# Kernel optimization log

Measured on AMD Instinct MI355X. Metric: run time of the kernel, lower is better.

The kernel has to match this reference:

```python
import jax, jax.numpy as jnp
import numpy as np

N_NODES = 50000
N_EDGES = 800000
VOCAB = 32000
IN_FEATS = 128
N_HIDDEN = 128
N_CLASSES = 40
SEQ_LEN = 20
PAD_IX = 0


def setup_inputs() -> dict:
    key = jax.random.key(0)
    ks = jax.random.split(key, 6)
    features = jax.random.randint(ks[0], (N_NODES, SEQ_LEN), 0, VOCAB, dtype=jnp.int64 if jax.config.jax_enable_x64 else jnp.int32).astype(jnp.int32)
    src = jax.random.randint(ks[1], (N_EDGES,), 0, N_NODES, dtype=jnp.int32)
    dst = jax.random.randint(ks[2], (N_EDGES,), 0, N_NODES, dtype=jnp.int32)
    emb_weight = jax.random.normal(ks[3], (VOCAB, IN_FEATS), dtype=jnp.float32) * 0.02
    emb_weight = emb_weight.at[PAD_IX].set(0.0)  # padding_idx row is zero
    W1 = jax.random.normal(ks[4], (IN_FEATS, N_HIDDEN), dtype=jnp.float32) * (1.0 / np.sqrt(IN_FEATS))
    b1 = jnp.zeros((N_HIDDEN,), dtype=jnp.float32)
    W2 = jax.random.normal(ks[5], (N_HIDDEN, N_CLASSES), dtype=jnp.float32) * (1.0 / np.sqrt(N_HIDDEN))
    b2 = jnp.zeros((N_CLASSES,), dtype=jnp.float32)
    return {"features": features, "src": src, "dst": dst, "emb_weight": emb_weight,
            "W1": W1, "b1": b1, "W2": W2, "b2": b2}


def _graph_conv(h, src, dst, W, b, n_nodes, activation=None):
    # DGL GraphConv with norm='both': D_out^{-1/2} applied to src feats,
    # sum-aggregate along edges, D_in^{-1/2} on dst, then linear (+bias, act).
    ones = jnp.ones(src.shape[0], dtype=h.dtype)
    out_deg = jax.ops.segment_sum(ones, src, num_segments=n_nodes)
    in_deg = jax.ops.segment_sum(ones, dst, num_segments=n_nodes)
    h = h * jax.lax.rsqrt(jnp.maximum(out_deg, 1.0))[:, None]
    agg = jax.ops.segment_sum(h[src], dst, num_segments=n_nodes)  # gather + scatter-add (SpMM)
    agg = agg * jax.lax.rsqrt(jnp.maximum(in_deg, 1.0))[:, None]
    out = agg @ W + b
    if activation is not None:
        out = activation(out)
    return out


def reference(features, src, dst, emb_weight, W1, b1, W2, b2):
    n_nodes = features.shape[0]
    # embedding mean-pool over non-pad tokens: [n_nodes, seq, d] -> [n_nodes, d]
    seq_len = jnp.maximum(jnp.sum(features != PAD_IX, axis=1, keepdims=True), 1).astype(emb_weight.dtype)
    h = jnp.take(emb_weight, features, axis=0).sum(axis=1) / seq_len
    h = _graph_conv(h, src, dst, W1, b1, n_nodes, activation=jax.nn.relu)
    # dropout is identity in eval mode
    h = _graph_conv(h, src, dst, W2, b2, n_nodes)
    return h
```

## Files before the change

### kernel.cpp

```cpp
#include <hip/hip_runtime.h>
#include <math.h>

#define N_NODES 50000
#define N_EDGES 800000
#define IN_FEATS 128
#define N_HIDDEN 128
#define N_CLASSES 40
#define SEQ_LEN 20
#define VOCAB 32000
#define BUCKET_CAP 64

#define NPART 196
#define PCAP 4608
#define EGS_BLOCKS 892
#define POOL_BLOCKS 12500
#define PREP_BLOCKS 89
#define GEMM2_BLOCKS 782

typedef __attribute__((ext_vector_type(8))) short bf16x8;
typedef __attribute__((ext_vector_type(4))) float f32x4;

#define AS1 __attribute__((address_space(1)))
#define AS3 __attribute__((address_space(3)))

__device__ __forceinline__ void gld_lds16(const void* g, void* l) {
    __builtin_amdgcn_global_load_lds((const AS1 unsigned int*)g,
                                     (AS3 unsigned int*)l, 16, 0, 0);
}
__device__ __forceinline__ void vm_wait0() {
    asm volatile("s_waitcnt vmcnt(0)" ::: "memory");
}

__device__ inline unsigned short f2bf(float x) {
    union { float f; unsigned int u; } v; v.f = x;
    unsigned int r = v.u + 0x7FFF + ((v.u >> 16) & 1);
    return (unsigned short)(r >> 16);
}
__device__ inline float bf2f(unsigned short b) {
    union { float f; unsigned int u; } v; v.u = ((unsigned int)b) << 16;
    return v.f;
}


__global__ __launch_bounds__(256) void prep_kernel(
        int4* __restrict__ pcnt_zero, const float* __restrict__ W1,
        unsigned short* __restrict__ W1p, const float* __restrict__ W2,
        unsigned short* __restrict__ W2p) {
    int b = blockIdx.x;
    int t = threadIdx.x;
    if (b == 0) {
        if (t < 128) pcnt_zero[t] = make_int4(0, 0, 0, 0);
    } else if (b < 65) {
        int i = (b - 1) * 256 + t;
        int tile = i >> 9, rem = i & 511;
        int ln = rem >> 3, j = rem & 7;
        int nt = tile >> 2, kb = tile & 3;
        int k = kb * 32 + ((ln >> 4) << 3) + j;
        int n = nt * 16 + (ln & 15);
        W1p[i] = f2bf(W1[k * 128 + n]);
    } else {
        int i = (b - 65) * 256 + t;
        int tile = i >> 9, rem = i & 511;
        int ln = rem >> 3, j = rem & 7;
        int nt = tile >> 2, kb = tile & 3;
        int k = kb * 32 + ((ln >> 4) << 3) + j;
        int n = nt * 16 + (ln & 15);
        W2p[i] = (n < N_CLASSES) ? f2bf(W2[k * N_CLASSES + n]) : (unsigned short)0;
    }
}

__global__ __launch_bounds__(256) void egemm_scat_kernel(
        const int* __restrict__ src, const int* __restrict__ dst,
        unsigned int* __restrict__ pcnt_s, unsigned char* __restrict__ pbuf_s,
        unsigned int* __restrict__ pcnt_d, unsigned int* __restrict__ pbuf_d,
        const float* __restrict__ emb, const unsigned short* __restrict__ W1p,
        unsigned short* __restrict__ Ep) {
    __shared__ unsigned int shm[512];
    int b = blockIdx.x;
    int t = threadIdx.x;
    if (b < 196) {
        unsigned int* lhist = shm;
        unsigned int* lbase = shm + 256;
        for (int i = t; i < NPART; i += 256) lhist[i] = 0u;
        __syncthreads();
        int base = b * 4096;
        int pid[16]; unsigned int rank[16]; unsigned char val[16];
        #pragma unroll
        for (int k = 0; k < 16; ++k) {
            int i = base + k * 256 + t;
            pid[k] = -1;
            if (i < N_EDGES) {
                int u = src[i];
                val[k] = (unsigned char)(u & 255);
                pid[k] = u >> 8;
                rank[k] = atomicAdd(&lhist[pid[k]], 1u);
            }
        }
        __syncthreads();
        for (int i = t; i < NPART; i += 256)
            lbase[i] = atomicAdd(&pcnt_s[i], lhist[i]);
        __syncthreads();
        #pragma unroll
        for (int k = 0; k < 16; ++k) {
            if (pid[k] >= 0) {
                unsigned int pos = lbase[pid[k]] + rank[k];
                if (pos < PCAP) pbuf_s[pid[k] * PCAP + pos] = val[k];
            }
        }
    } else if (b < 392) {
        unsigned int* lhist = shm;
        unsigned int* lbase = shm + 256;
        for (int i = t; i < NPART; i += 256) lhist[i] = 0u;
        __syncthreads();
        int base = (b - 196) * 4096;
        int pid[16]; unsigned int rank[16]; unsigned int val[16];
        #pragma unroll
        for (int k = 0; k < 16; ++k) {
            int i = base + k * 256 + t;
            pid[k] = -1;
            if (i < N_EDGES) {
                int u = src[i];
                int d = dst[i];
                val[k] = ((unsigned int)u << 8) | (unsigned int)(d & 255);
                pid[k] = d >> 8;
                rank[k] = atomicAdd(&lhist[pid[k]], 1u);
            }
        }
        __syncthreads();
        for (int i = t; i < NPART; i += 256)
            lbase[i] = atomicAdd(&pcnt_d[i], lhist[i]);
        __syncthreads();
        #pragma unroll
        for (int k = 0; k < 16; ++k) {
            if (pid[k] >= 0) {
                unsigned int pos = lbase[pid[k]] + rank[k];
                if (pos < PCAP) pbuf_d[pid[k] * PCAP + pos] = val[k];
            }
        }
    } else {
        const int wave = t >> 6, lane = t & 63;
        const int quad = lane >> 4, m = lane & 15;
        const int row0 = (b - 392) * 64 + wave * 16;
        const int arow = row0 + m;
        const float4* ap = (const float4*)(emb + arow * 128 + quad * 8);
        bf16x8 a[4];
        #pragma unroll
        for (int kb = 0; kb < 4; ++kb) {
            float4 x = ap[kb * 8];
            float4 y = ap[kb * 8 + 1];
            bf16x8 tt;
            tt[0] = f2bf(x.x); tt[1] = f2bf(x.y); tt[2] = f2bf(x.z); tt[3] = f2bf(x.w);
            tt[4] = f2bf(y.x); tt[5] = f2bf(y.y); tt[6] = f2bf(y.z); tt[7] = f2bf(y.w);
            a[kb] = tt;
        }
        const int rbase = row0 + quad * 4;
        #pragma unroll
        for (int nt = 0; nt < 8; ++nt) {
            const unsigned short* wp = W1p + (nt * 4) * 512 + lane * 8;
            bf16x8 b0 = *(const bf16x8*)(wp + 0 * 512);
            bf16x8 b1 = *(const bf16x8*)(wp + 1 * 512);
            bf16x8 b2 = *(const bf16x8*)(wp + 2 * 512);
            bf16x8 b3 = *(const bf16x8*)(wp + 3 * 512);
            f32x4 acc = {0.f, 0.f, 0.f, 0.f};
            acc = __builtin_amdgcn_mfma_f32_16x16x32_bf16(a[0], b0, acc, 0, 0, 0);
            acc = __builtin_amdgcn_mfma_f32_16x16x32_bf16(a[1], b1, acc, 0, 0, 0);
            acc = __builtin_amdgcn_mfma_f32_16x16x32_bf16(a[2], b2, acc, 0, 0, 0);
            acc = __builtin_amdgcn_mfma_f32_16x16x32_bf16(a[3], b3, acc, 0, 0, 0);
            #pragma unroll
            for (int r = 0; r < 4; ++r)
                Ep[(rbase + r) * 128 + nt * 16 + m] = f2bf(acc[r]);
        }
    }
}

__global__ __launch_bounds__(256) void count_kernel(
        const unsigned int* __restrict__ pcnt_s, const unsigned char* __restrict__ pbuf_s,
        const unsigned int* __restrict__ pcnt_d, const unsigned int* __restrict__ pbuf_d,
        unsigned int* __restrict__ cnt, float* __restrict__ routf,
        unsigned short* __restrict__ bucketu) {
    __shared__ unsigned int ho[256];
    __shared__ unsigned int hi_[256];
    int p = blockIdx.x, t = threadIdx.x;
    ho[t] = 0u;
    hi_[t] = 0u;
    __syncthreads();
    int ns = min((int)pcnt_s[p], PCAP);
    const unsigned char* ps = pbuf_s + p * PCAP;
    for (int i = t; i < ns; i += 256) atomicAdd(&ho[ps[i]], 1u);
    int nd = min((int)pcnt_d[p], PCAP);
    const unsigned int* pd = pbuf_d + p * PCAP;
    for (int i = t; i < nd; i += 256) {
        unsigned int e = pd[i];
        unsigned int d = e & 255u;
        unsigned int slot = atomicAdd(&hi_[d], 1u);
        if (slot < BUCKET_CAP)
            bucketu[(p * 256 + (int)d) * BUCKET_CAP + slot] = (unsigned short)(e >> 8);
    }
    __syncthreads();
    int v = p * 256 + t;
    if (v < N_NODES) {
        cnt[v] = (ho[t] << 16) | (hi_[t] & 0xffffu);
        routf[v] = rsqrtf(fmaxf((float)ho[t], 1.f));
    }
}

__global__ __launch_bounds__(256) void pool_kernel(
        const float* __restrict__ routf, const int* __restrict__ feats,
        const unsigned short* __restrict__ Ep, unsigned short* __restrict__ G1) {
    __shared__ unsigned int pstage[4][SEQ_LEN][64];
    __shared__ int tokl[4][SEQ_LEN];
    int t = threadIdx.x;
    int w = t >> 6, lane = t & 63;
    int v = blockIdx.x * 4 + w;
    int mytok = 0;
    if (lane < SEQ_LEN) {
        mytok = feats[v * SEQ_LEN + lane];
        tokl[w][lane] = mytok;
    }
    int nz = (int)__popcll(__ballot(lane < SEQ_LEN && mytok != 0));
    __syncthreads();
    #pragma unroll
    for (int g = 0; g < SEQ_LEN / 4; ++g) {
        int tok = tokl[w][4 * g + (lane >> 4)];
        gld_lds16(Ep + tok * 128 + (lane & 15) * 8, &pstage[w][4 * g][0]);
    }
    float ro = routf[v];
    vm_wait0();
    float a0 = 0.f, a1 = 0.f;
    #pragma unroll
    for (int s = 0; s < SEQ_LEN; ++s) {
        unsigned int x = pstage[w][s][lane];
        a0 += bf2f((unsigned short)(x & 0xffffu));
        a1 += bf2f((unsigned short)(x >> 16));
    }
    float sc = ro / (float)max(nz, 1);
    ushort2 o = {f2bf(a0 * sc), f2bf(a1 * sc)};
    ((ushort2*)G1)[v * 64 + lane] = o;
}

__global__ __launch_bounds__(256) void spmm1_kernel(
        const unsigned int* __restrict__ cnt, const float* __restrict__ routf,
        const unsigned short* __restrict__ bucketu, const unsigned short* __restrict__ G,
        const float* __restrict__ b1, unsigned short* __restrict__ h1) {
    __shared__ unsigned short idxs[256];
    __shared__ unsigned int stg[4][32][64];
    int t = threadIdx.x;
    int node = t >> 6, lane = t & 63;
    int v = blockIdx.x * 4 + node;
    idxs[t] = bucketu[blockIdx.x * 256 + t];
    int ind = (int)(cnt[v] & 0xffffu);
    float rov = routf[v];
    float2 bb = ((const float2*)b1)[lane];
    int n = min(ind, BUCKET_CAP);
    float a0 = 0.f, a1 = 0.f;
    for (int base = 0; base < n; base += 32) {
        int m = min(32, n - base);
        int nin = (m + 3) >> 2;
        for (int g = 0; g < nin; ++g) {
            int rc = min(base + 4 * g + (lane >> 4), n - 1);
            int u = idxs[node * 64 + rc];
            gld_lds16(G + u * 128 + (lane & 15) * 8, &stg[node][4 * g][0]);
        }
        vm_wait0();
        #pragma unroll 4
        for (int j = 0; j < m; ++j) {
            unsigned int x = stg[node][j][lane];
            a0 += bf2f((unsigned short)(x & 0xffffu));
            a1 += bf2f((unsigned short)(x >> 16));
        }
    }
    float rin = rsqrtf(fmaxf((float)ind, 1.f));
    float v0 = fmaxf(a0 * rin + bb.x, 0.f) * rov;
    float v1 = fmaxf(a1 * rin + bb.y, 0.f) * rov;
    ushort2 o = {f2bf(v0), f2bf(v1)};
    ((ushort2*)h1)[v * 64 + lane] = o;
}

__global__ __launch_bounds__(256) void gemm2_kernel(
        const unsigned short* __restrict__ h1, const unsigned short* __restrict__ W2p,
        unsigned short* __restrict__ G2) {
    const int wave = threadIdx.x >> 6, lane = threadIdx.x & 63;
    const int quad = lane >> 4, m = lane & 15;
    const int row0 = blockIdx.x * 64 + wave * 16;
    const int arow = min(row0 + m, N_NODES - 1);
    const unsigned short* ap = h1 + arow * 128 + quad * 8;
    bf16x8 a0 = *(const bf16x8*)(ap + 0);
    bf16x8 a1 = *(const bf16x8*)(ap + 32);
    bf16x8 a2 = *(const bf16x8*)(ap + 64);
    bf16x8 a3 = *(const bf16x8*)(ap + 96);
    const int rbase = row0 + quad * 4;
    #pragma unroll
    for (int nt = 0; nt < 3; ++nt) {
        const unsigned short* wp = W2p + (nt * 4) * 512 + lane * 8;
        bf16x8 b0 = *(const bf16x8*)(wp + 0 * 512);
        bf16x8 b1 = *(const bf16x8*)(wp + 1 * 512);
        bf16x8 b2 = *(const bf16x8*)(wp + 2 * 512);
        bf16x8 b3 = *(const bf16x8*)(wp + 3 * 512);
        f32x4 acc = {0.f, 0.f, 0.f, 0.f};
        acc = __builtin_amdgcn_mfma_f32_16x16x32_bf16(a0, b0, acc, 0, 0, 0);
        acc = __builtin_amdgcn_mfma_f32_16x16x32_bf16(a1, b1, acc, 0, 0, 0);
        acc = __builtin_amdgcn_mfma_f32_16x16x32_bf16(a2, b2, acc, 0, 0, 0);
        acc = __builtin_amdgcn_mfma_f32_16x16x32_bf16(a3, b3, acc, 0, 0, 0);
        int col = nt * 16 + m;
        #pragma unroll
        for (int r = 0; r < 4; ++r) {
            int row = rbase + r;
            if (row < N_NODES && col < N_CLASSES)
                G2[row * 64 + col] = f2bf(acc[r]);
        }
    }
}

__global__ __launch_bounds__(256) void spmm2_kernel(
        const unsigned int* __restrict__ cnt, const unsigned short* __restrict__ bucketu,
        const unsigned short* __restrict__ G2, const float* __restrict__ b2,
        float* __restrict__ out) {
    __shared__ unsigned short idxs[256];
    __shared__ unsigned short stg[4][32][64];
    int t = threadIdx.x;
    int node = t >> 6, f = t & 63;
    int v = blockIdx.x * 4 + node;
    idxs[t] = bucketu[blockIdx.x * 256 + t];
    int ind = (int)(cnt[v] & 0xffffu);
    int n = min(ind, BUCKET_CAP);
    float acc = 0.f;
    for (int base = 0; base < n; base += 32) {
        int m = min(32, n - base);
        int nin = (m + 7) >> 3;
        for (int g = 0; g < nin; ++g) {
            int rc = min(base + 8 * g + (f >> 3), n - 1);
            int u = idxs[node * 64 + rc];
            gld_lds16(G2 + u * 64 + (f & 7) * 8, &stg[node][8 * g][0]);
        }
        vm_wait0();
        if (f < N_CLASSES) {
            #pragma unroll 4
            for (int j = 0; j < m; ++j) acc += bf2f(stg[node][j][f]);
        }
    }
    if (f < N_CLASSES) {
        float rin = rsqrtf(fmaxf((float)ind, 1.f));
        out[v * N_CLASSES + f] = acc * rin + b2[f];
    }
}

extern "C" void kernel_launch(void* const* d_in, const int* in_sizes, int n_in,
                              void* d_out, int out_size, void* d_ws, size_t ws_size,
                              hipStream_t stream) {
    const int*   feats = (const int*)d_in[0];
    const int*   src   = (const int*)d_in[1];
    const int*   dst   = (const int*)d_in[2];
    const float* emb   = (const float*)d_in[3];
    const float* W1    = (const float*)d_in[4];
    const float* b1    = (const float*)d_in[5];
    const float* W2    = (const float*)d_in[6];
    const float* b2    = (const float*)d_in[7];
    float* out = (float*)d_out;

    char* w = (char*)d_ws;
    unsigned int*   cnt     = (unsigned int*)(w + 0);
    unsigned int*   pcnt_s  = (unsigned int*)(w + 200704);
    unsigned int*   pcnt_d  = (unsigned int*)(w + 201728);
    float*          routf   = (float*)(w + 202752);
    unsigned short* bucketu = (unsigned short*)(w + 403456);
    unsigned char*  pbuf_s  = (unsigned char*)(w + 6803456);
    unsigned int*   pbuf_d  = (unsigned int*)(w + 7706624);
    unsigned short* Ep      = (unsigned short*)(w + 11319296);
    unsigned short* h1      = (unsigned short*)(w + 6803456);
    unsigned short* G1      = (unsigned short*)(w + 19603456);
    unsigned short* G2      = (unsigned short*)(w + 32403456);
    unsigned short* W1p     = (unsigned short*)(w + 38803456);
    unsigned short* W2p     = (unsigned short*)(w + 38836224);

    prep_kernel<<<PREP_BLOCKS, 256, 0, stream>>>((int4*)pcnt_s, W1, W1p, W2, W2p);
    egemm_scat_kernel<<<EGS_BLOCKS, 256, 0, stream>>>(
        src, dst, pcnt_s, pbuf_s, pcnt_d, pbuf_d, emb, W1p, Ep);
    count_kernel<<<NPART, 256, 0, stream>>>(
        pcnt_s, pbuf_s, pcnt_d, pbuf_d, cnt, routf, bucketu);
    pool_kernel<<<POOL_BLOCKS, 256, 0, stream>>>(routf, feats, Ep, G1);
    spmm1_kernel<<<POOL_BLOCKS, 256, 0, stream>>>(cnt, routf, bucketu, G1, b1, h1);
    gemm2_kernel<<<GEMM2_BLOCKS, 256, 0, stream>>>(h1, W2p, G2);
    spmm2_kernel<<<POOL_BLOCKS, 256, 0, stream>>>(cnt, bucketu, G2, b2, out);
}
```

Measured before the change: 190.8 us.

## Merge degree counting with embedding pooling and move out-degree scaling into SpMM1

```diff
diff --git a/kernel.cpp b/kernel.cpp
--- a/kernel.cpp
+++ b/kernel.cpp
@@ -14,6 +14,7 @@
 #define PCAP 4608
 #define EGS_BLOCKS 892
 #define POOL_BLOCKS 12500
+#define POOLCOUNT_BLOCKS (NPART + POOL_BLOCKS)
 #define PREP_BLOCKS 89
 #define GEMM2_BLOCKS 782
 
@@ -173,45 +174,46 @@
     }
 }
 
-__global__ __launch_bounds__(256) void count_kernel(
+__global__ __launch_bounds__(256) void poolcount_kernel(
         const unsigned int* __restrict__ pcnt_s, const unsigned char* __restrict__ pbuf_s,
         const unsigned int* __restrict__ pcnt_d, const unsigned int* __restrict__ pbuf_d,
         unsigned int* __restrict__ cnt, float* __restrict__ routf,
-        unsigned short* __restrict__ bucketu) {
-    __shared__ unsigned int ho[256];
-    __shared__ unsigned int hi_[256];
-    int p = blockIdx.x, t = threadIdx.x;
-    ho[t] = 0u;
-    hi_[t] = 0u;
-    __syncthreads();
-    int ns = min((int)pcnt_s[p], PCAP);
-    const unsigned char* ps = pbuf_s + p * PCAP;
-    for (int i = t; i < ns; i += 256) atomicAdd(&ho[ps[i]], 1u);
-    int nd = min((int)pcnt_d[p], PCAP);
-    const unsigned int* pd = pbuf_d + p * PCAP;
-    for (int i = t; i < nd; i += 256) {
-        unsigned int e = pd[i];
-        unsigned int d = e & 255u;
-        unsigned int slot = atomicAdd(&hi_[d], 1u);
-        if (slot < BUCKET_CAP)
-            bucketu[(p * 256 + (int)d) * BUCKET_CAP + slot] = (unsigned short)(e >> 8);
-    }
-    __syncthreads();
-    int v = p * 256 + t;
-    if (v < N_NODES) {
-        cnt[v] = (ho[t] << 16) | (hi_[t] & 0xffffu);
-        routf[v] = rsqrtf(fmaxf((float)ho[t], 1.f));
-    }
-}
-
-__global__ __launch_bounds__(256) void pool_kernel(
-        const float* __restrict__ routf, const int* __restrict__ feats,
-        const unsigned short* __restrict__ Ep, unsigned short* __restrict__ G1) {
-    __shared__ unsigned int pstage[4][SEQ_LEN][64];
+        unsigned short* __restrict__ bucketu,
+        const int* __restrict__ feats, const unsigned short* __restrict__ Ep,
+        unsigned short* __restrict__ G1) {
+    __shared__ unsigned int shm[4][SEQ_LEN][64];
     __shared__ int tokl[4][SEQ_LEN];
-    int t = threadIdx.x;
+    int b = blockIdx.x;
+    int t = threadIdx.x;
+    if (b < NPART) {
+        unsigned int* ho = &shm[0][0][0];
+        unsigned int* hi_ = &shm[0][0][0] + 256;
+        ho[t] = 0u;
+        hi_[t] = 0u;
+        __syncthreads();
+        int p = b;
+        int ns = min((int)pcnt_s[p], PCAP);
+        const unsigned char* ps = pbuf_s + p * PCAP;
+        for (int i = t; i < ns; i += 256) atomicAdd(&ho[ps[i]], 1u);
+        int nd = min((int)pcnt_d[p], PCAP);
+        const unsigned int* pd = pbuf_d + p * PCAP;
+        for (int i = t; i < nd; i += 256) {
+            unsigned int e = pd[i];
+            unsigned int d = e & 255u;
+            unsigned int slot = atomicAdd(&hi_[d], 1u);
+            if (slot < BUCKET_CAP)
+                bucketu[(p * 256 + (int)d) * BUCKET_CAP + slot] = (unsigned short)(e >> 8);
+        }
+        __syncthreads();
+        int v = p * 256 + t;
+        if (v < N_NODES) {
+            cnt[v] = (ho[t] << 16) | (hi_[t] & 0xffffu);
+            routf[v] = rsqrtf(fmaxf((float)ho[t], 1.f));
+        }
+        return;
+    }
     int w = t >> 6, lane = t & 63;
-    int v = blockIdx.x * 4 + w;
+    int v = (b - NPART) * 4 + w;
     int mytok = 0;
     if (lane < SEQ_LEN) {
         mytok = feats[v * SEQ_LEN + lane];
@@ -222,18 +224,17 @@
     #pragma unroll
     for (int g = 0; g < SEQ_LEN / 4; ++g) {
         int tok = tokl[w][4 * g + (lane >> 4)];
-        gld_lds16(Ep + tok * 128 + (lane & 15) * 8, &pstage[w][4 * g][0]);
-    }
-    float ro = routf[v];
+        gld_lds16(Ep + tok * 128 + (lane & 15) * 8, &shm[w][4 * g][0]);
+    }
     vm_wait0();
     float a0 = 0.f, a1 = 0.f;
     #pragma unroll
     for (int s = 0; s < SEQ_LEN; ++s) {
-        unsigned int x = pstage[w][s][lane];
+        unsigned int x = shm[w][s][lane];
         a0 += bf2f((unsigned short)(x & 0xffffu));
         a1 += bf2f((unsigned short)(x >> 16));
     }
-    float sc = ro / (float)max(nz, 1);
+    float sc = 1.f / (float)max(nz, 1);
     ushort2 o = {f2bf(a0 * sc), f2bf(a1 * sc)};
     ((ushort2*)G1)[v * 64 + lane] = o;
 }
@@ -243,35 +244,42 @@
         const unsigned short* __restrict__ bucketu, const unsigned short* __restrict__ G,
         const float* __restrict__ b1, unsigned short* __restrict__ h1) {
     __shared__ unsigned short idxs[256];
-    __shared__ unsigned int stg[4][32][64];
+    __shared__ unsigned int stg[4][16][64];
     int t = threadIdx.x;
     int node = t >> 6, lane = t & 63;
     int v = blockIdx.x * 4 + node;
     idxs[t] = bucketu[blockIdx.x * 256 + t];
     int ind = (int)(cnt[v] & 0xffffu);
-    float rov = routf[v];
+    float rovv = routf[v];
     float2 bb = ((const float2*)b1)[lane];
     int n = min(ind, BUCKET_CAP);
+    const unsigned short* bk = &idxs[node * 64];
     float a0 = 0.f, a1 = 0.f;
-    for (int base = 0; base < n; base += 32) {
-        int m = min(32, n - base);
+    for (int base = 0; base < n; base += 16) {
+        int m = min(16, n - base);
         int nin = (m + 3) >> 2;
         for (int g = 0; g < nin; ++g) {
             int rc = min(base + 4 * g + (lane >> 4), n - 1);
-            int u = idxs[node * 64 + rc];
+            int u = bk[rc];
             gld_lds16(G + u * 128 + (lane & 15) * 8, &stg[node][4 * g][0]);
         }
+        float rv[16];
+        #pragma unroll
+        for (int j = 0; j < 16; ++j)
+            rv[j] = routf[bk[base + min(j, m - 1)]];
         vm_wait0();
-        #pragma unroll 4
-        for (int j = 0; j < m; ++j) {
-            unsigned int x = stg[node][j][lane];
-            a0 += bf2f((unsigned short)(x & 0xffffu));
-            a1 += bf2f((unsigned short)(x >> 16));
+        #pragma unroll
+        for (int j = 0; j < 16; ++j) {
+            if (j < m) {
+                unsigned int x = stg[node][j][lane];
+                a0 += bf2f((unsigned short)(x & 0xffffu)) * rv[j];
+                a1 += bf2f((unsigned short)(x >> 16)) * rv[j];
+            }
         }
     }
     float rin = rsqrtf(fmaxf((float)ind, 1.f));
-    float v0 = fmaxf(a0 * rin + bb.x, 0.f) * rov;
-    float v1 = fmaxf(a1 * rin + bb.y, 0.f) * rov;
+    float v0 = fmaxf(a0 * rin + bb.x, 0.f) * rovv;
+    float v1 = fmaxf(a1 * rin + bb.y, 0.f) * rovv;
     ushort2 o = {f2bf(v0), f2bf(v1)};
     ((ushort2*)h1)[v * 64 + lane] = o;
 }
@@ -375,9 +383,8 @@
     prep_kernel<<<PREP_BLOCKS, 256, 0, stream>>>((int4*)pcnt_s, W1, W1p, W2, W2p);
     egemm_scat_kernel<<<EGS_BLOCKS, 256, 0, stream>>>(
         src, dst, pcnt_s, pbuf_s, pcnt_d, pbuf_d, emb, W1p, Ep);
-    count_kernel<<<NPART, 256, 0, stream>>>(
-        pcnt_s, pbuf_s, pcnt_d, pbuf_d, cnt, routf, bucketu);
-    pool_kernel<<<POOL_BLOCKS, 256, 0, stream>>>(routf, feats, Ep, G1);
+    poolcount_kernel<<<POOLCOUNT_BLOCKS, 256, 0, stream>>>(
+        pcnt_s, pbuf_s, pcnt_d, pbuf_d, cnt, routf, bucketu, feats, Ep, G1);
     spmm1_kernel<<<POOL_BLOCKS, 256, 0, stream>>>(cnt, routf, bucketu, G1, b1, h1);
     gemm2_kernel<<<GEMM2_BLOCKS, 256, 0, stream>>>(h1, W2p, G2);
     spmm2_kernel<<<POOL_BLOCKS, 256, 0, stream>>>(cnt, bucketu, G2, b2, out);
```

After: 185.5 us (median of 2 runs). 1.03x faster.
